# Kernel tuning notes

Measured on AMD Instinct MI355X. Metric: run time of the kernel, lower is better.

## Reference

```python
import jax, jax.numpy as jnp
import numpy as np

B = 4096; T = 2; S = 4; E = 128; NF = 11; ID = 55; MID = 4; NG = 6; SI = 4
EPS = 1e-5

def _bn(x, axis):
    # BatchNorm in training mode at init (gamma=1, beta=0): normalize over batch axis
    m = jnp.mean(x, axis=axis, keepdims=True)
    v = jnp.var(x, axis=axis, keepdims=True)
    return (x - m) * jax.lax.rsqrt(v + EPS)

def setup_inputs() -> dict:
    key = jax.random.key(0)
    keys = iter(jax.random.split(key, 64))
    def n(shape, s=0.05):
        return jax.random.normal(next(keys), shape, dtype=jnp.float32) * s
    cat = jax.random.randint(next(keys), (B, 9), 0, 1000)
    scen = jax.random.randint(next(keys), (B, 1), 0, S)
    return {
        "categorical_x": jnp.concatenate([scen, cat], axis=1).astype(jnp.int32),
        "numerical_x": n((B, 63), 1.0),
        "emb_table": n((9000, E)), "lin_table": n((9000, E)),
        "user_W": n((E, 23)), "user_b": n((E,)), "item_W": n((E, 40)), "item_b": n((E,)),
        "user_lW": n((E, 23)), "user_lb": n((E,)), "item_lW": n((E, 40)), "item_lb": n((E,)),
        "scen_emb": n((S, SI)), "task_emb": n((T, SI)),
        "st_w": n((T, S, 1)), "interact_w": n((1, ID, 1)),
        "sb_W": n((14, E)), "sb_b": n((14,)), "lsb_W": n((14, E)), "lsb_b": n((14,)),
        "shexp_W": n((4, MID, 14)), "shexp_b": n((4, MID)),
        "spexp_W": n((S, T, 2, MID, 14)), "spexp_b": n((S, T, 2, MID)),
        "lshexp_W": n((4, MID, 14)), "lshexp_b": n((4, MID)),
        "lspexp_W": n((S, T, 2, MID, 14)), "lspexp_b": n((S, T, 2, MID)),
        "gate_W": n((S, T, NG, SI + E)), "gate_b": n((S, T, NG)),
        "lgate_W": n((S, T, NG, SI + E)), "lgate_b": n((S, T, NG)),
        "mask_W": n((S, T, ID, ID * MID)), "mask_b": n((S, T, ID)),
        "att_W": n((S, T, ID)),
        "ltower_W": n((S, T, NF, NF * MID)), "ltower_b": n((S, T, NF)),
        "bias_p": n((T, S, E)),
        "last_W1": n((T, 40, 2 * E)), "last_b1": n((T, 40)),
        "last_W2": n((T, 32, 40)), "last_b2": n((T, 32)),
        "last_W3": n((T, 8, 32)), "last_b3": n((T, 8)),
        "last_W4": n((T, 1, 8)), "last_b4": n((T, 1)),
    }

def _fwd(categorical_x, numerical_x, emb_table, lin_table, user_W, user_b, item_W, item_b,
         user_lW, user_lb, item_lW, item_lb, scen_emb, task_emb, st_w, interact_w,
         sb_W, sb_b, lsb_W, lsb_b, shexp_W, shexp_b, spexp_W, spexp_b,
         lshexp_W, lshexp_b, lspexp_W, lspexp_b, gate_W, gate_b, lgate_W, lgate_b,
         mask_W, mask_b, att_W, ltower_W, ltower_b, bias_p,
         last_W1, last_b1, last_W2, last_b2, last_W3, last_b3, last_W4, last_b4):
    b = categorical_x.shape[0]
    scen_ids = categorical_x[:, 0]
    onehot = jax.nn.one_hot(scen_ids, S, dtype=jnp.float32)                 # [B,S]
    scen_ind = scen_emb[scen_ids]                                           # [B,SI]
    stw = jnp.einsum('bs,tso->bt', onehot, st_w)                            # [B,T]
    sti = scen_ind[:, None, :] * task_emb[None] * stw[:, :, None]           # [B,T,SI]

    offsets = (jnp.arange(9) * 1000).astype(categorical_x.dtype)
    idx = categorical_x[:, 1:] + offsets                                    # [B,9]

    def fields_of(table, uW, ub, iW, ib):
        ce = table[idx]                                                     # [B,9,E]
        u = (numerical_x[:, :23] @ uW.T + ub)[:, None, :]
        it = (numerical_x[:, 23:] @ iW.T + ib)[:, None, :]
        return jnp.concatenate([ce, u, it], axis=1)                          # [B,NF,E]

    def moe(x, att_in, sbW, sbb, shW, shb, spW, spb, gW, gb):
        # x: [B,F,E]; att_in: [B,T,F,SI+E] -> soft-routed expert mix [S,T,B,F,MID]
        ein = x @ sbW.T + sbb                                                # [B,F,14]
        sh = jnp.einsum('bfi,eoi->ebfo', ein, shW) + shb[:, None, None, :]   # [4,B,F,MID]
        sp = jnp.einsum('bfi,steoi->stebfo', ein, spW) + spb[:, :, :, None, None, :]
        experts = jnp.concatenate(
            [jnp.broadcast_to(sh[None, None], (S, T) + sh.shape), sp], axis=2)  # [S,T,NG,B,F,MID]
        g = jax.nn.softmax(jnp.einsum('btfi,stgi->stbfg', att_in, gW) + gb[:, :, None, None, :], axis=-1)
        return jnp.einsum('stgbfm,stbfg->stbfm', experts, g)

    # ---- interaction (FM pairwise) branch ----
    fields = fields_of(emb_table, user_W, user_b, item_W, item_b)
    r, c = jnp.triu_indices(NF, k=1)
    pe = fields[:, r, :] * fields[:, c, :] * interact_w                     # [B,ID,E]
    att_in_pe = jnp.concatenate([
        jnp.broadcast_to(sti[:, :, None, :], (b, T, ID, SI)),
        jnp.broadcast_to(pe[:, None], (b, T, ID, E))], axis=-1)             # [B,T,ID,SI+E]
    w = moe(pe, att_in_pe, sb_W, sb_b, shexp_W, shexp_b, spexp_W, spexp_b, gate_W, gate_b)
    m = jnp.einsum('stbi,stoi->stbo', w.reshape(S, T, b, ID * MID), mask_W) + mask_b[:, :, None, :]
    m = jax.nn.relu(jnp.tanh(_bn(m, axis=2)))                               # hard-sparse mask [S,T,B,ID]
    att_out = jnp.einsum('stbf,bfe,stf->stbe', m, pe, att_W)                # [S,T,B,E]
    inter = jnp.einsum('bs,stbe->tbe', onehot, att_out)                     # select own scenario [T,B,E]

    # ---- linear (first-order) branch ----
    lfields = fields_of(lin_table, user_lW, user_lb, item_lW, item_lb)      # [B,NF,E]
    att_in_l = jnp.concatenate([
        jnp.broadcast_to(sti[:, :, None, :], (b, T, NF, SI)),
        jnp.broadcast_to(lfields[:, None], (b, T, NF, E))], axis=-1)
    w2 = moe(lfields, att_in_l, lsb_W, lsb_b, lshexp_W, lshexp_b, lspexp_W, lspexp_b, lgate_W, lgate_b)
    lt = jnp.einsum('stbi,stoi->stbo', w2.reshape(S, T, b, NF * MID), ltower_W) + ltower_b[:, :, None, :]
    lt = jax.nn.softmax(_bn(lt, axis=2), axis=-1)                           # field weights [S,T,B,NF]
    lw = jnp.einsum('bs,stbf->tbf', onehot, lt)
    lin_final = jnp.einsum('tbf,bfe->tbe', lw, lfields) + jnp.einsum('bs,tse->tbe', onehot, bias_p)

    # ---- per-task output towers ----
    h = jnp.concatenate([inter, lin_final], axis=-1)                        # [T,B,2E]
    h = jax.nn.relu(_bn(jnp.einsum('tbi,toi->tbo', h, last_W1) + last_b1[:, None, :], axis=1))
    h = jax.nn.relu(_bn(jnp.einsum('tbi,toi->tbo', h, last_W2) + last_b2[:, None, :], axis=1))
    h = jax.nn.relu(_bn(jnp.einsum('tbi,toi->tbo', h, last_W3) + last_b3[:, None, :], axis=1))
    out = jax.nn.sigmoid(jnp.einsum('tbi,toi->tbo', h, last_W4) + last_b4[:, None, :])
    return out[..., 0]                                                      # [T,B]

def reference(categorical_x, numerical_x, emb_table, lin_table, user_W, user_b, item_W, item_b,
              user_lW, user_lb, item_lW, item_lb, scen_emb, task_emb, st_w, interact_w,
              sb_W, sb_b, lsb_W, lsb_b, shexp_W, shexp_b, spexp_W, spexp_b,
              lshexp_W, lshexp_b, lspexp_W, lspexp_b, gate_W, gate_b, lgate_W, lgate_b,
              mask_W, mask_b, att_W, ltower_W, ltower_b, bias_p,
              last_W1, last_b1, last_W2, last_b2, last_W3, last_b3, last_W4, last_b4):
    return _fwd(categorical_x, numerical_x, emb_table, lin_table, user_W, user_b, item_W, item_b,
                user_lW, user_lb, item_lW, item_lb, scen_emb, task_emb, st_w, interact_w,
                sb_W, sb_b, lsb_W, lsb_b, shexp_W, shexp_b, spexp_W, spexp_b,
                lshexp_W, lshexp_b, lspexp_W, lspexp_b, gate_W, gate_b, lgate_W, lgate_b,
                mask_W, mask_b, att_W, ltower_W, ltower_b, bias_p,
                last_W1, last_b1, last_W2, last_b2, last_W3, last_b3, last_W4, last_b4)
```

## Files before the change

### kernel.cpp

```cpp
#include <hip/hip_runtime.h>
#include <hip/hip_bf16.h>

#define B_ 4096
#define T_ 2
#define S_ 4
#define E_ 128
#define NF_ 11
#define ID_ 55
#define MID_ 4
#define NG_ 6
#define SI_ 4
#define EPSf 1e-5f

typedef __attribute__((ext_vector_type(8))) short bf16x8;
typedef __attribute__((ext_vector_type(4))) float f32x4;

__device__ inline unsigned short f2bf(float f){
  unsigned int u = __float_as_uint(f);
  unsigned int r = (u + 0x7FFFu + ((u >> 16) & 1u)) >> 16;
  return (unsigned short)r;
}

__device__ const int PR[64]={0,0,0,0,0,0,0,0,0,0,1,1,1,1,1,1,1,1,1,2,2,2,2,2,2,2,2,3,3,3,3,3,3,3,4,4,4,4,4,4,5,5,5,5,5,6,6,6,6,7,7,7,8,8,9,0,0,0,0,0,0,0,0,0};
__device__ const int PC[64]={1,2,3,4,5,6,7,8,9,10,2,3,4,5,6,7,8,9,10,3,4,5,6,7,8,9,10,4,5,6,7,8,9,10,5,6,7,8,9,10,6,7,8,9,10,7,8,9,10,8,9,10,9,10,10,0,0,0,0,0,0,0,0,0};

__global__ void k_prep(const float* __restrict__ gW, const float* __restrict__ lgW,
                       const float* __restrict__ sbW, const float* __restrict__ lsbW,
                       float* __restrict__ Wu, float* __restrict__ lWu,
                       unsigned short* __restrict__ Wub){
  int k = blockIdx.x*256 + threadIdx.x;
  if (k < 16384){
    int arr = k >> 13, rem = k & 8191;
    int o = rem >> 7, e = rem & 127;
    const float* g = arr ? lgW : gW;
    const float* s = arr ? lsbW : sbW;
    float v;
    if (o < 48) v = g[o*132 + 4 + e];
    else if (o < 62) v = s[(o-48)*128 + e];
    else v = 0.f;
    (arr ? lWu : Wu)[o*128 + e] = v;
  }
  if (k < 64*136){
    int o = k / 136, e = k % 136;
    float v = 0.f;
    if (e < 128){
      if (o < 48) v = gW[o*132 + 4 + e];
      else if (o < 62) v = sbW[(o-48)*128 + e];
    }
    Wub[k] = f2bf(v);
  }
}

__global__ __launch_bounds__(256) void k_moe12(
    const int* __restrict__ cat, const float* __restrict__ num,
    const float* __restrict__ embT, const float* __restrict__ linT,
    const float* __restrict__ uW, const float* __restrict__ ub,
    const float* __restrict__ iW, const float* __restrict__ ib,
    const float* __restrict__ ulW, const float* __restrict__ ulb,
    const float* __restrict__ ilW, const float* __restrict__ ilb,
    const float* __restrict__ scen_emb, const float* __restrict__ task_emb,
    const float* __restrict__ st_w, const float* __restrict__ interact_w,
    const float* __restrict__ sb_b,
    const float* __restrict__ shexp_W, const float* __restrict__ shexp_b,
    const float* __restrict__ spexp_W, const float* __restrict__ spexp_b,
    const float* __restrict__ gate_W, const float* __restrict__ gate_b,
    const unsigned short* __restrict__ Wub,
    const float* __restrict__ lsb_b,
    const float* __restrict__ lshexp_W, const float* __restrict__ lshexp_b,
    const float* __restrict__ lspexp_W, const float* __restrict__ lspexp_b,
    const float* __restrict__ lgate_W, const float* __restrict__ lgate_b,
    const float* __restrict__ ltower_W, const float* __restrict__ ltower_b,
    const float* __restrict__ lWu,
    float* __restrict__ w_g, float* __restrict__ lt1)
{
  __shared__ float sm[9592];
  float* s_fld = sm;
  float* s_stig= sm + 1452;
  unsigned short* s_peb = (unsigned short*)(sm + 1500);
  unsigned short* s_wub = (unsigned short*)(sm + 5240);
  float* s_C   = sm + 1500;
  float* s_w   = sm + 5916;
  float* s_sh  = sm + 7676;
  float* s_lf   = sm + 5916;
  float* m2_w   = sm + 7676;
  float* m2_sh  = sm + 8028;
  float* m2_C   = sm + 8611;
  float* m2_stig= sm + 9439;
  const int tid = threadIdx.x, b = blockIdx.x;
  const int* cb = cat + (size_t)b*10;
  const int scen = cb[0];
  const int e = tid & 127, half = tid >> 7;

  if (half == 0){
    for (int j = 0; j < 9; j += 2){
      int id = cb[1+j] + j*1000;
      s_fld[j*132 + e] = embT[(size_t)id*128 + e];
    }
    float a0 = ub[e];
    for (int k = 0; k < 23; ++k) a0 += num[(size_t)b*63 + k] * uW[e*23 + k];
    s_fld[9*132 + e] = a0;
  } else {
    for (int j = 1; j < 9; j += 2){
      int id = cb[1+j] + j*1000;
      s_fld[j*132 + e] = embT[(size_t)id*128 + e];
    }
    float a2 = ib[e];
    for (int k = 0; k < 40; ++k) a2 += num[(size_t)b*63 + 23 + k] * iW[e*40 + k];
    s_fld[10*132 + e] = a2;
  }
  for (int idx = tid; idx < 1088; idx += 256)
    ((float4*)s_wub)[idx] = ((const float4*)Wub)[idx];
  if (tid < 48){
    int t = (tid/6)%T_;
    float stw = st_w[t*S_ + scen];
    float acc = gate_b[tid];
    for (int i = 0; i < 4; ++i){
      float sti = scen_emb[scen*4+i] * task_emb[t*4+i] * stw;
      acc += sti * gate_W[tid*132 + i];
    }
    s_stig[tid] = acc;
  }
  __syncthreads();

  for (int idx = tid; idx < 1760; idx += 256){
    int row = idx >> 5, q = idx & 31;
    float4 x = *(const float4*)&s_fld[PR[row]*132 + q*4];
    float4 y = *(const float4*)&s_fld[PC[row]*132 + q*4];
    ushort4 o;
    o.x = f2bf(x.x*y.x); o.y = f2bf(x.y*y.y); o.z = f2bf(x.z*y.z); o.w = f2bf(x.w*y.w);
    *(ushort4*)&s_peb[row*136 + q*4] = o;
  }
  __syncthreads();

  const int w = tid >> 6, lane = tid & 63;
  const int cg = lane >> 4, cc = lane & 15;
  f32x4 acc0 = {0.f,0.f,0.f,0.f}, acc1 = acc0, acc2 = acc0, acc3 = acc0;
  {
    const int kb = cg * 8;
    #pragma unroll
    for (int ks = 0; ks < 4; ++ks){
      int ko = ks*32 + kb;
      bf16x8 bfr = *(const bf16x8*)&s_wub[(w*16 + cc)*136 + ko];
      bf16x8 a0 = *(const bf16x8*)&s_peb[( 0 + cc)*136 + ko];
      bf16x8 a1 = *(const bf16x8*)&s_peb[(16 + cc)*136 + ko];
      bf16x8 a2 = *(const bf16x8*)&s_peb[(32 + cc)*136 + ko];
      bf16x8 a3 = *(const bf16x8*)&s_peb[(48 + cc)*136 + ko];
      acc0 = __builtin_amdgcn_mfma_f32_16x16x32_bf16(a0, bfr, acc0, 0, 0, 0);
      acc1 = __builtin_amdgcn_mfma_f32_16x16x32_bf16(a1, bfr, acc1, 0, 0, 0);
      acc2 = __builtin_amdgcn_mfma_f32_16x16x32_bf16(a2, bfr, acc2, 0, 0, 0);
      acc3 = __builtin_amdgcn_mfma_f32_16x16x32_bf16(a3, bfr, acc3, 0, 0, 0);
    }
  }
  __syncthreads();
  {
    const int col = w*16 + cc;
    const float bias = (col < 48) ? s_stig[col] : ((col < 62) ? sb_b[col-48] : 0.f);
    #pragma unroll
    for (int r = 0; r < 4; ++r){
      int row0 = cg*4 + r;
      float v0 = (r==0)?acc0.x:((r==1)?acc0.y:((r==2)?acc0.z:acc0.w));
      float v1 = (r==0)?acc1.x:((r==1)?acc1.y:((r==2)?acc1.z:acc1.w));
      float v2 = (r==0)?acc2.x:((r==1)?acc2.y:((r==2)?acc2.z:acc2.w));
      float v3 = (r==0)?acc3.x:((r==1)?acc3.y:((r==2)?acc3.z:acc3.w));
      s_C[(row0     )*69 + col] = v0*interact_w[row0     ] + bias;
      s_C[(row0 + 16)*69 + col] = v1*interact_w[row0 + 16] + bias;
      s_C[(row0 + 32)*69 + col] = v2*interact_w[row0 + 32] + bias;
      if (row0 + 48 < 55)
        s_C[(row0 + 48)*69 + col] = v3*interact_w[row0 + 48] + bias;
    }
  }
  __syncthreads();
  for (int o = tid; o < 880; o += 256){
    int f = o >> 4, j = o & 15;
    float acc = shexp_b[j];
    const float* ein = &s_C[f*69 + 48];
    const float* wp = &shexp_W[j*14];
    for (int i = 0; i < 14; ++i) acc += ein[i] * wp[i];
    s_sh[f*17 + j] = acc;
  }
  __syncthreads();
  for (int task = tid; task < 440; task += 256){
    int st = task / 55, f = task % 55;
    float ein[14];
    for (int i = 0; i < 14; ++i) ein[i] = s_C[f*69 + 48 + i];
    float lg[6], mx = -1e30f;
    for (int g = 0; g < 6; ++g){ lg[g] = s_C[f*69 + st*6 + g]; mx = fmaxf(mx, lg[g]); }
    float sum = 0.f;
    for (int g = 0; g < 6; ++g){ lg[g] = __expf(lg[g]-mx); sum += lg[g]; }
    float inv = 1.f/sum;
    float wv[4] = {0,0,0,0};
    for (int g = 0; g < 4; ++g){
      float gg = lg[g]*inv;
      for (int m = 0; m < 4; ++m) wv[m] += gg * s_sh[f*17 + g*4 + m];
    }
    for (int ee = 0; ee < 2; ++ee){
      float gg = lg[4+ee]*inv;
      for (int m = 0; m < 4; ++m){
        float acc = spexp_b[(st*2+ee)*4+m];
        const float* wp = spexp_W + ((st*2+ee)*4+m)*14;
        for (int i = 0; i < 14; ++i) acc += ein[i] * wp[i];
        wv[m] += gg*acc;
      }
    }
    float4 o4; o4.x = wv[0]; o4.y = wv[1]; o4.z = wv[2]; o4.w = wv[3];
    *(float4*)&s_w[st*220 + f*4] = o4;
  }
  __syncthreads();
  for (int idx = tid; idx < 448; idx += 256){
    int st = idx / 56, q = idx % 56;
    float4 v;
    if (q < 55) v = *(float4*)&s_w[st*220 + q*4];
    else { v.x=v.y=v.z=v.w=0.f; }
    *(float4*)&w_g[((size_t)b*8 + st)*224 + q*4] = v;
  }
  __syncthreads();

  if (half == 0){
    for (int j = 0; j < 9; j += 2){
      int id = cb[1+j] + j*1000;
      s_lf[j*132 + e] = linT[(size_t)id*128 + e];
    }
    float a1 = ulb[e];
    for (int k = 0; k < 23; ++k) a1 += num[(size_t)b*63 + k] * ulW[e*23 + k];
    s_lf[9*132 + e] = a1;
  } else {
    for (int j = 1; j < 9; j += 2){
      int id = cb[1+j] + j*1000;
      s_lf[j*132 + e] = linT[(size_t)id*128 + e];
    }
    float a3 = ilb[e];
    for (int k = 0; k < 40; ++k) a3 += num[(size_t)b*63 + 23 + k] * ilW[e*40 + k];
    s_lf[10*132 + e] = a3;
  }
  if (tid >= 224){
    int q = tid - 224;
    float4 z = {0,0,0,0}; *(float4*)&s_lf[11*132 + q*4] = z;
  }
  if (tid < 48){
    int t = (tid/6)%T_;
    float stw = st_w[t*S_ + scen];
    float acc = lgate_b[tid];
    for (int i = 0; i < 4; ++i){
      float sti = scen_emb[scen*4+i] * task_emb[t*4+i] * stw;
      acc += sti * lgate_W[tid*132 + i];
    }
    m2_stig[tid] = acc;
  }
  __syncthreads();
  {
    const int lane2 = tid & 63, wv_ = tid >> 6;
    const int pr = wv_*16 + (lane2 & 15);
    const int ks = lane2 >> 4;
    const int ft = pr & 1, ot = pr >> 1;
    const int r0 = ft*6, k0 = ks*32;
    float acc[6][2];
    for (int r = 0; r < 6; ++r){ acc[r][0] = 0.f; acc[r][1] = 0.f; }
    const float4* W4 = (const float4*)lWu;
    #pragma unroll 1
    for (int kc = 0; kc < 32; kc += 4){
      int kk = k0 + ((kc + ks*8) & 31);
      float4 w0 = W4[(ot*2+0)*32 + (kk>>2)];
      float4 w1 = W4[(ot*2+1)*32 + (kk>>2)];
      for (int r = 0; r < 6; ++r){
        float4 a = *(const float4*)&s_lf[(r0+r)*132 + kk];
        acc[r][0] += a.x*w0.x + a.y*w0.y + a.z*w0.z + a.w*w0.w;
        acc[r][1] += a.x*w1.x + a.y*w1.y + a.z*w1.z + a.w*w1.w;
      }
    }
    for (int r = 0; r < 6; ++r) for (int c = 0; c < 2; ++c){
      float v = acc[r][c];
      v += __shfl_xor(v, 16); v += __shfl_xor(v, 32);
      acc[r][c] = v;
    }
    if (ks == 0){
      for (int r = 0; r < 6; ++r) for (int c = 0; c < 2; ++c){
        int col = ot*2 + c, row = r0 + r;
        float bias = (col < 48) ? m2_stig[col] : ((col < 62) ? lsb_b[col-48] : 0.f);
        m2_C[row*69 + col] = acc[r][c] + bias;
      }
    }
  }
  __syncthreads();
  if (tid < 176){
    int f = tid >> 4, j = tid & 15;
    float acc = lshexp_b[j];
    const float* ein = &m2_C[f*69 + 48];
    for (int i = 0; i < 14; ++i) acc += ein[i] * lshexp_W[j*14+i];
    m2_sh[f*17 + j] = acc;
  }
  __syncthreads();
  if (tid < 88){
    int st = tid / 11, f = tid % 11;
    float ein[14];
    for (int i = 0; i < 14; ++i) ein[i] = m2_C[f*69 + 48 + i];
    float lg[6], mx = -1e30f;
    for (int g = 0; g < 6; ++g){ lg[g] = m2_C[f*69 + st*6 + g]; mx = fmaxf(mx, lg[g]); }
    float sum = 0.f;
    for (int g = 0; g < 6; ++g){ lg[g] = __expf(lg[g]-mx); sum += lg[g]; }
    float inv = 1.f/sum;
    float wv[4] = {0,0,0,0};
    for (int g = 0; g < 4; ++g){
      float gg = lg[g]*inv;
      for (int m = 0; m < 4; ++m) wv[m] += gg * m2_sh[f*17 + g*4 + m];
    }
    for (int ee = 0; ee < 2; ++ee){
      float gg = lg[4+ee]*inv;
      for (int m = 0; m < 4; ++m){
        float acc = lspexp_b[(st*2+ee)*4+m];
        const float* wp = lspexp_W + ((st*2+ee)*4+m)*14;
        for (int i = 0; i < 14; ++i) acc += ein[i] * wp[i];
        wv[m] += gg*acc;
      }
    }
    float4 o4; o4.x = wv[0]; o4.y = wv[1]; o4.z = wv[2]; o4.w = wv[3];
    *(float4*)&m2_w[st*44 + f*4] = o4;
  }
  __syncthreads();
  if (tid < 88){
    int st = tid / 11, oo = tid % 11;
    float acc = ltower_b[st*11+oo];
    const float* tw = ltower_W + (st*11+oo)*44;
    const float* wp = m2_w + st*44;
    for (int i = 0; i < 44; ++i) acc += wp[i] * tw[i];
    lt1[(size_t)(st*11+oo)*B_ + b] = acc;
  }
}

__global__ __launch_bounds__(256) void k_mask(
    const float* __restrict__ w_g, const float* __restrict__ mask_W,
    const float* __restrict__ mask_b, float* __restrict__ m1)
{
  __shared__ float s_mw[56*116];
  __shared__ float s_wb[64*116];
  const int tid = threadIdx.x;
  const int st = blockIdx.x >> 6, bt = blockIdx.x & 63;
  const int b0 = bt*64;
  const int btl = tid & 15, ot = tid >> 4;
  float acc[4][4];
  for (int c = 0; c < 4; ++c) for (int j = 0; j < 4; ++j) acc[c][j] = 0.f;

  for (int kc = 0; kc < 2; ++kc){
    __syncthreads();
    for (int idx = tid; idx < 64*112; idx += 256){
      int r = idx / 112, k = idx % 112;
      s_wb[r*116 + k] = w_g[((size_t)(b0+r)*8 + st)*224 + kc*112 + k];
    }
    for (int idx = tid; idx < 56*112; idx += 256){
      int r = idx / 112, k = idx % 112;
      int kg = kc*112 + k;
      s_mw[r*116 + k] = (r < 55 && kg < 220) ? mask_W[((size_t)st*55 + r)*220 + kg] : 0.f;
    }
    __syncthreads();
    if (ot < 14){
      for (int k4 = 0; k4 < 112; k4 += 4){
        float4 a[4], wb[4];
        for (int c = 0; c < 4; ++c) a[c]  = *(float4*)&s_mw[(ot*4+c)*116 + k4];
        for (int j = 0; j < 4; ++j) wb[j] = *(float4*)&s_wb[(btl*4+j)*116 + k4];
        for (int c = 0; c < 4; ++c)
          for (int j = 0; j < 4; ++j)
            acc[c][j] += a[c].x*wb[j].x + a[c].y*wb[j].y + a[c].z*wb[j].z + a[c].w*wb[j].w;
      }
    }
  }
  if (ot < 14){
    for (int c = 0; c < 4; ++c){
      int row = ot*4 + c;
      if (row < 55){
        float mb = mask_b[st*55 + row];
        float4 v; v.x = acc[c][0]+mb; v.y = acc[c][1]+mb; v.z = acc[c][2]+mb; v.w = acc[c][3]+mb;
        *(float4*)&m1[(size_t)(st*55+row)*B_ + b0 + btl*4] = v;
      }
    }
  }
}

__global__ __launch_bounds__(256) void k_stats(const float* __restrict__ x, float* __restrict__ stats){
  const int row = blockIdx.x, tid = threadIdx.x;
  const float* xr = x + (size_t)row*B_;
  float s = 0.f, s2 = 0.f;
  for (int i = tid; i < B_; i += 256){ float v = xr[i]; s += v; s2 += v*v; }
  for (int off = 32; off > 0; off >>= 1){ s += __shfl_down(s, off); s2 += __shfl_down(s2, off); }
  __shared__ float red[8];
  if ((tid & 63) == 0){ red[(tid>>6)*2] = s; red[(tid>>6)*2+1] = s2; }
  __syncthreads();
  if (tid == 0){
    float Ssum = red[0]+red[2]+red[4]+red[6], S2 = red[1]+red[3]+red[5]+red[7];
    float mean = Ssum*(1.f/B_), var = S2*(1.f/B_) - mean*mean;
    stats[row*2] = mean; stats[row*2+1] = rsqrtf(fmaxf(var, 0.f) + EPSf);
  }
}

__global__ __launch_bounds__(256) void k_stats2(const float* __restrict__ x1, const float* __restrict__ x2,
                                                int n1, float* __restrict__ st1o, float* __restrict__ st2o){
  const int row = blockIdx.x, tid = threadIdx.x;
  const float* xr; float* sto;
  if (row < n1){ xr = x1 + (size_t)row*B_; sto = st1o + row*2; }
  else { int r = row - n1; xr = x2 + (size_t)r*B_; sto = st2o + r*2; }
  float s = 0.f, s2 = 0.f;
  for (int i = tid; i < B_; i += 256){ float v = xr[i]; s += v; s2 += v*v; }
  for (int off = 32; off > 0; off >>= 1){ s += __shfl_down(s, off); s2 += __shfl_down(s2, off); }
  __shared__ float red[8];
  if ((tid & 63) == 0){ red[(tid>>6)*2] = s; red[(tid>>6)*2+1] = s2; }
  __syncthreads();
  if (tid == 0){
    float Ssum = red[0]+red[2]+red[4]+red[6], S2 = red[1]+red[3]+red[5]+red[7];
    float mean = Ssum*(1.f/B_), var = S2*(1.f/B_) - mean*mean;
    sto[0] = mean; sto[1] = rsqrtf(fmaxf(var, 0.f) + EPSf);
  }
}

__global__ __launch_bounds__(128) void k_interlinf(
    const int* __restrict__ cat, const float* __restrict__ num,
    const float* __restrict__ embT, const float* __restrict__ linT,
    const float* __restrict__ uW, const float* __restrict__ ub,
    const float* __restrict__ iW, const float* __restrict__ ib,
    const float* __restrict__ ulW, const float* __restrict__ ulb,
    const float* __restrict__ ilW, const float* __restrict__ ilb,
    const float* __restrict__ m1, const float* __restrict__ stm,
    const float* __restrict__ lt1, const float* __restrict__ stl,
    const float* __restrict__ att_W, const float* __restrict__ interact_w,
    const float* __restrict__ bias_p,
    const float* __restrict__ W1, const float* __restrict__ b1,
    float* __restrict__ h1)
{
  __shared__ float s_fld[NF_*E_];
  __shared__ float s_lf[NF_*E_];
  __shared__ float s_co[110];
  __shared__ float s_lw[22];
  __shared__ float s_h[512];
  const int b = blockIdx.x, e = threadIdx.x;
  const int* cb = cat + (size_t)b*10;
  const int scen = cb[0];

  for (int j = 0; j < 9; ++j){
    int id = cb[1+j] + j*1000;
    s_fld[j*E_+e] = embT[(size_t)id*128 + e];
    s_lf[j*E_+e]  = linT[(size_t)id*128 + e];
  }
  {
    float a0 = ub[e], a1 = ulb[e];
    for (int k = 0; k < 23; ++k){ float x = num[(size_t)b*63 + k]; a0 += x*uW[e*23+k]; a1 += x*ulW[e*23+k]; }
    s_fld[9*E_+e] = a0; s_lf[9*E_+e] = a1;
    float a2 = ib[e], a3 = ilb[e];
    for (int k = 0; k < 40; ++k){ float x = num[(size_t)b*63 + 23 + k]; a2 += x*iW[e*40+k]; a3 += x*ilW[e*40+k]; }
    s_fld[10*E_+e] = a2; s_lf[10*E_+e] = a3;
  }
  if (e < 110){
    int t = e/55, f = e%55, row = (scen*T_+t)*55 + f;
    float v = (m1[(size_t)row*B_+b] - stm[row*2]) * stm[row*2+1];
    v = fmaxf(tanhf(v), 0.f);
    s_co[e] = v * att_W[(scen*T_+t)*55 + f];
  }
  if (e < 22){
    int t = e/11, f = e%11, row = (scen*T_+t)*11 + f;
    s_lw[e] = (lt1[(size_t)row*B_+b] - stl[row*2]) * stl[row*2+1];
  }
  __syncthreads();
  if (e < 2){
    int t = e; float mx = -1e30f;
    for (int f = 0; f < 11; ++f) mx = fmaxf(mx, s_lw[t*11+f]);
    float sum = 0.f;
    for (int f = 0; f < 11; ++f){ float x = __expf(s_lw[t*11+f]-mx); s_lw[t*11+f] = x; sum += x; }
    float inv = 1.f/sum;
    for (int f = 0; f < 11; ++f) s_lw[t*11+f] *= inv;
  }
  __syncthreads();
  {
    float a0 = 0.f, a1 = 0.f;
    for (int f = 0; f < 55; ++f){
      float pe = s_fld[PR[f]*E_+e] * s_fld[PC[f]*E_+e] * interact_w[f];
      a0 += s_co[f]*pe; a1 += s_co[55+f]*pe;
    }
    s_h[0*256 + e] = a0;
    s_h[1*256 + e] = a1;
  }
  for (int t = 0; t < 2; ++t){
    float acc = bias_p[(size_t)(t*S_+scen)*E_ + e];
    for (int f = 0; f < 11; ++f) acc += s_lw[t*11+f] * s_lf[f*E_+e];
    s_h[t*256 + 128 + e] = acc;
  }
  __syncthreads();
  if (e < 80){
    int t = e / 40, o = e % 40;
    float acc = b1[t*40 + o];
    const float4* wr = (const float4*)(W1 + (size_t)(t*40 + o)*256);
    const float4* hh = (const float4*)(s_h + t*256);
    for (int i = 0; i < 64; ++i){
      float4 w = wr[i], h = hh[i];
      acc += h.x*w.x; acc += h.y*w.y; acc += h.z*w.z; acc += h.w*w.w;
    }
    h1[(size_t)(t*40 + o)*B_ + b] = acc;
  }
}

__global__ __launch_bounds__(256) void k_last2(const float* __restrict__ h1, const float* __restrict__ st1,
    const float* __restrict__ W2, const float* __restrict__ b2v, float* __restrict__ h2){
  int bz = blockIdx.x, t = bz/16, bc = bz%16, tid = threadIdx.x, b = bc*256 + tid;
  __shared__ float s_w2[1280];
  for (int k = tid; k < 1280; k += 256) s_w2[k] = W2[t*1280 + k];
  __syncthreads();
  float hv[40];
  for (int i = 0; i < 40; ++i){
    int row = t*40 + i;
    hv[i] = fmaxf((h1[(size_t)row*B_+b] - st1[row*2]) * st1[row*2+1], 0.f);
  }
  for (int o = 0; o < 32; ++o){
    float acc = b2v[t*32+o];
    for (int i = 0; i < 40; ++i) acc += hv[i] * s_w2[o*40+i];
    h2[(size_t)(t*32+o)*B_ + b] = acc;
  }
}

__global__ __launch_bounds__(256) void k_last3(const float* __restrict__ h2, const float* __restrict__ st2,
    const float* __restrict__ W3, const float* __restrict__ b3v, float* __restrict__ h3){
  int bz = blockIdx.x, t = bz/16, bc = bz%16, tid = threadIdx.x, b = bc*256 + tid;
  __shared__ float s_w3[256];
  if (tid < 256) s_w3[tid] = W3[t*256 + tid];
  __syncthreads();
  float hv[32];
  for (int i = 0; i < 32; ++i){
    int row = t*32 + i;
    hv[i] = fmaxf((h2[(size_t)row*B_+b] - st2[row*2]) * st2[row*2+1], 0.f);
  }
  for (int o = 0; o < 8; ++o){
    float acc = b3v[t*8+o];
    for (int i = 0; i < 32; ++i) acc += hv[i] * s_w3[o*32+i];
    h3[(size_t)(t*8+o)*B_ + b] = acc;
  }
}

__global__ __launch_bounds__(256) void k_out(const float* __restrict__ h3, const float* __restrict__ st3,
    const float* __restrict__ W4, const float* __restrict__ b4v, float* __restrict__ out){
  int idx = blockIdx.x*256 + threadIdx.x;
  int t = idx / B_, b = idx % B_;
  float acc = b4v[t];
  for (int i = 0; i < 8; ++i){
    int row = t*8 + i;
    float v = fmaxf((h3[(size_t)row*B_+b] - st3[row*2]) * st3[row*2+1], 0.f);
    acc += v * W4[t*8+i];
  }
  out[idx] = 1.f/(1.f + __expf(-acc));
}

extern "C" void kernel_launch(void* const* d_in, const int* in_sizes, int n_in,
                              void* d_out, int out_size, void* d_ws, size_t ws_size,
                              hipStream_t stream)
{
  const int*   cat      = (const int*)  d_in[0];
  const float* num      = (const float*)d_in[1];
  const float* embT     = (const float*)d_in[2];
  const float* linT     = (const float*)d_in[3];
  const float* uW = (const float*)d_in[4];  const float* ub = (const float*)d_in[5];
  const float* iW = (const float*)d_in[6];  const float* ib = (const float*)d_in[7];
  const float* ulW = (const float*)d_in[8]; const float* ulb = (const float*)d_in[9];
  const float* ilW = (const float*)d_in[10];const float* ilb = (const float*)d_in[11];
  const float* scen_emb = (const float*)d_in[12];
  const float* task_emb = (const float*)d_in[13];
  const float* st_w     = (const float*)d_in[14];
  const float* interact_w=(const float*)d_in[15];
  const float* sbW = (const float*)d_in[16]; const float* sbb = (const float*)d_in[17];
  const float* lsbW = (const float*)d_in[18];const float* lsbb = (const float*)d_in[19];
  const float* shW = (const float*)d_in[20]; const float* shb = (const float*)d_in[21];
  const float* spW = (const float*)d_in[22]; const float* spb = (const float*)d_in[23];
  const float* lshW = (const float*)d_in[24];const float* lshb = (const float*)d_in[25];
  const float* lspW = (const float*)d_in[26];const float* lspb = (const float*)d_in[27];
  const float* gW = (const float*)d_in[28];  const float* gb = (const float*)d_in[29];
  const float* lgW = (const float*)d_in[30]; const float* lgb = (const float*)d_in[31];
  const float* mW = (const float*)d_in[32];  const float* mb = (const float*)d_in[33];
  const float* attW = (const float*)d_in[34];
  const float* ltW = (const float*)d_in[35]; const float* ltb = (const float*)d_in[36];
  const float* biasP = (const float*)d_in[37];
  const float* W1 = (const float*)d_in[38];  const float* b1 = (const float*)d_in[39];
  const float* W2 = (const float*)d_in[40];  const float* b2v = (const float*)d_in[41];
  const float* W3 = (const float*)d_in[42];  const float* b3v = (const float*)d_in[43];
  const float* W4 = (const float*)d_in[44];  const float* b4v = (const float*)d_in[45];
  float* out = (float*)d_out;

  float* ws = (float*)d_ws;
  size_t o = 0;
  float* Wu   = ws + o; o += 8192;
  float* lWu  = ws + o; o += 8192;
  float* Wub  = ws + o; o += 4352;
  float* w_g  = ws + o; o += (size_t)B_*8*224;
  float* m1   = ws + o; o += (size_t)440*B_;
  float* stm  = ws + o; o += 880;
  float* lt1  = ws + o; o += (size_t)88*B_;
  float* stl  = ws + o; o += 176;
  float* h1   = ws + o; o += (size_t)80*B_;
  float* st1  = ws + o; o += 160;
  float* h2   = ws + o; o += (size_t)64*B_;
  float* st2  = ws + o; o += 128;
  float* h3   = ws + o; o += (size_t)16*B_;
  float* st3  = ws + o; o += 32;

  k_prep<<<64, 256, 0, stream>>>(gW, lgW, sbW, lsbW, Wu, lWu, (unsigned short*)Wub);
  k_moe12<<<B_, 256, 0, stream>>>(cat, num, embT, linT, uW, ub, iW, ib, ulW, ulb, ilW, ilb,
                                  scen_emb, task_emb, st_w, interact_w, sbb, shW, shb,
                                  spW, spb, gW, gb, (const unsigned short*)Wub,
                                  lsbb, lshW, lshb, lspW, lspb, lgW, lgb, ltW, ltb,
                                  lWu, w_g, lt1);
  k_mask<<<512, 256, 0, stream>>>(w_g, mW, mb, m1);
  k_stats2<<<528, 256, 0, stream>>>(m1, lt1, 440, stm, stl);
  k_interlinf<<<B_, 128, 0, stream>>>(cat, num, embT, linT, uW, ub, iW, ib, ulW, ulb, ilW, ilb,
                                      m1, stm, lt1, stl, attW, interact_w, biasP,
                                      W1, b1, h1);
  k_stats<<<80, 256, 0, stream>>>(h1, st1);
  k_last2<<<32, 256, 0, stream>>>(h1, st1, W2, b2v, h2);
  k_stats<<<64, 256, 0, stream>>>(h2, st2);
  k_last3<<<32, 256, 0, stream>>>(h2, st2, W3, b3v, h3);
  k_stats<<<16, 256, 0, stream>>>(h3, st3);
  k_out<<<32, 256, 0, stream>>>(h3, st3, W4, b4v, out);
}
```

Before: 448.4 us.

## Use bf16 MFMA for linear-branch gate GEMM and shrink shared memory

The second (linear-feature) gate/sub-bias projection now runs on bf16 MFMA with prepacked bf16 weights instead of fp32 scalar dot products. Weight tiles are read directly from global/L2 rather than staged in LDS. The shared-memory footprint drops, with a tighter C stride and w_g written straight to global, to raise occupancy. The cost is reduced precision in the linear branch, since both its features and weights are now bf16, and uncached weight reads in the MFMA loop.

Result: faster. 402.7 us (-10.2%).

```diff
diff --git a/kernel.cpp b/kernel.cpp
--- a/kernel.cpp
+++ b/kernel.cpp
@@ -26,28 +26,17 @@
 
 __global__ void k_prep(const float* __restrict__ gW, const float* __restrict__ lgW,
                        const float* __restrict__ sbW, const float* __restrict__ lsbW,
-                       float* __restrict__ Wu, float* __restrict__ lWu,
-                       unsigned short* __restrict__ Wub){
+                       unsigned short* __restrict__ Wub, unsigned short* __restrict__ lWub){
   int k = blockIdx.x*256 + threadIdx.x;
-  if (k < 16384){
-    int arr = k >> 13, rem = k & 8191;
-    int o = rem >> 7, e = rem & 127;
-    const float* g = arr ? lgW : gW;
-    const float* s = arr ? lsbW : sbW;
-    float v;
-    if (o < 48) v = g[o*132 + 4 + e];
-    else if (o < 62) v = s[(o-48)*128 + e];
-    else v = 0.f;
-    (arr ? lWu : Wu)[o*128 + e] = v;
-  }
-  if (k < 64*136){
+  if (k < 8704){
     int o = k / 136, e = k % 136;
-    float v = 0.f;
+    float v = 0.f, lv = 0.f;
     if (e < 128){
-      if (o < 48) v = gW[o*132 + 4 + e];
-      else if (o < 62) v = sbW[(o-48)*128 + e];
+      if (o < 48){ v = gW[o*132 + 4 + e]; lv = lgW[o*132 + 4 + e]; }
+      else if (o < 62){ v = sbW[(o-48)*128 + e]; lv = lsbW[(o-48)*128 + e]; }
     }
     Wub[k] = f2bf(v);
+    lWub[k] = f2bf(lv);
   }
 }
 
@@ -70,26 +59,26 @@
     const float* __restrict__ lspexp_W, const float* __restrict__ lspexp_b,
     const float* __restrict__ lgate_W, const float* __restrict__ lgate_b,
     const float* __restrict__ ltower_W, const float* __restrict__ ltower_b,
-    const float* __restrict__ lWu,
+    const unsigned short* __restrict__ lWub,
     float* __restrict__ w_g, float* __restrict__ lt1)
 {
-  __shared__ float sm[9592];
+  __shared__ float sm[6595];
   float* s_fld = sm;
   float* s_stig= sm + 1452;
   unsigned short* s_peb = (unsigned short*)(sm + 1500);
-  unsigned short* s_wub = (unsigned short*)(sm + 5240);
   float* s_C   = sm + 1500;
-  float* s_w   = sm + 5916;
-  float* s_sh  = sm + 7676;
-  float* s_lf   = sm + 5916;
-  float* m2_w   = sm + 7676;
-  float* m2_sh  = sm + 8028;
-  float* m2_C   = sm + 8611;
-  float* m2_stig= sm + 9439;
+  float* s_sh  = sm + 5660;
+  unsigned short* s_lfb = (unsigned short*)(sm + 1500);
+  float* m2_C   = sm + 2588;
+  float* m2_sh  = sm + 3368;
+  float* m2_stig= sm + 3555;
+  float* m2_w   = sm + 3603;
   const int tid = threadIdx.x, b = blockIdx.x;
   const int* cb = cat + (size_t)b*10;
   const int scen = cb[0];
   const int e = tid & 127, half = tid >> 7;
+  const int w = tid >> 6, lane = tid & 63;
+  const int cg = lane >> 4, cc = lane & 15;
 
   if (half == 0){
     for (int j = 0; j < 9; j += 2){
@@ -108,8 +97,6 @@
     for (int k = 0; k < 40; ++k) a2 += num[(size_t)b*63 + 23 + k] * iW[e*40 + k];
     s_fld[10*132 + e] = a2;
   }
-  for (int idx = tid; idx < 1088; idx += 256)
-    ((float4*)s_wub)[idx] = ((const float4*)Wub)[idx];
   if (tid < 48){
     int t = (tid/6)%T_;
     float stw = st_w[t*S_ + scen];
@@ -132,15 +119,13 @@
   }
   __syncthreads();
 
-  const int w = tid >> 6, lane = tid & 63;
-  const int cg = lane >> 4, cc = lane & 15;
   f32x4 acc0 = {0.f,0.f,0.f,0.f}, acc1 = acc0, acc2 = acc0, acc3 = acc0;
   {
     const int kb = cg * 8;
     #pragma unroll
     for (int ks = 0; ks < 4; ++ks){
       int ko = ks*32 + kb;
-      bf16x8 bfr = *(const bf16x8*)&s_wub[(w*16 + cc)*136 + ko];
+      bf16x8 bfr = *(const bf16x8*)&Wub[(w*16 + cc)*136 + ko];
       bf16x8 a0 = *(const bf16x8*)&s_peb[( 0 + cc)*136 + ko];
       bf16x8 a1 = *(const bf16x8*)&s_peb[(16 + cc)*136 + ko];
       bf16x8 a2 = *(const bf16x8*)&s_peb[(32 + cc)*136 + ko];
@@ -162,18 +147,18 @@
       float v1 = (r==0)?acc1.x:((r==1)?acc1.y:((r==2)?acc1.z:acc1.w));
       float v2 = (r==0)?acc2.x:((r==1)?acc2.y:((r==2)?acc2.z:acc2.w));
       float v3 = (r==0)?acc3.x:((r==1)?acc3.y:((r==2)?acc3.z:acc3.w));
-      s_C[(row0     )*69 + col] = v0*interact_w[row0     ] + bias;
-      s_C[(row0 + 16)*69 + col] = v1*interact_w[row0 + 16] + bias;
-      s_C[(row0 + 32)*69 + col] = v2*interact_w[row0 + 32] + bias;
+      s_C[(row0     )*65 + col] = v0*interact_w[row0     ] + bias;
+      s_C[(row0 + 16)*65 + col] = v1*interact_w[row0 + 16] + bias;
+      s_C[(row0 + 32)*65 + col] = v2*interact_w[row0 + 32] + bias;
       if (row0 + 48 < 55)
-        s_C[(row0 + 48)*69 + col] = v3*interact_w[row0 + 48] + bias;
+        s_C[(row0 + 48)*65 + col] = v3*interact_w[row0 + 48] + bias;
     }
   }
   __syncthreads();
   for (int o = tid; o < 880; o += 256){
     int f = o >> 4, j = o & 15;
     float acc = shexp_b[j];
-    const float* ein = &s_C[f*69 + 48];
+    const float* ein = &s_C[f*65 + 48];
     const float* wp = &shexp_W[j*14];
     for (int i = 0; i < 14; ++i) acc += ein[i] * wp[i];
     s_sh[f*17 + j] = acc;
@@ -182,9 +167,9 @@
   for (int task = tid; task < 440; task += 256){
     int st = task / 55, f = task % 55;
     float ein[14];
-    for (int i = 0; i < 14; ++i) ein[i] = s_C[f*69 + 48 + i];
+    for (int i = 0; i < 14; ++i) ein[i] = s_C[f*65 + 48 + i];
     float lg[6], mx = -1e30f;
-    for (int g = 0; g < 6; ++g){ lg[g] = s_C[f*69 + st*6 + g]; mx = fmaxf(mx, lg[g]); }
+    for (int g = 0; g < 6; ++g){ lg[g] = s_C[f*65 + st*6 + g]; mx = fmaxf(mx, lg[g]); }
     float sum = 0.f;
     for (int g = 0; g < 6; ++g){ lg[g] = __expf(lg[g]-mx); sum += lg[g]; }
     float inv = 1.f/sum;
@@ -203,38 +188,30 @@
       }
     }
     float4 o4; o4.x = wv[0]; o4.y = wv[1]; o4.z = wv[2]; o4.w = wv[3];
-    *(float4*)&s_w[st*220 + f*4] = o4;
-  }
-  __syncthreads();
-  for (int idx = tid; idx < 448; idx += 256){
-    int st = idx / 56, q = idx % 56;
-    float4 v;
-    if (q < 55) v = *(float4*)&s_w[st*220 + q*4];
-    else { v.x=v.y=v.z=v.w=0.f; }
-    *(float4*)&w_g[((size_t)b*8 + st)*224 + q*4] = v;
+    *(float4*)&w_g[((size_t)b*8 + st)*224 + f*4] = o4;
+  }
+  if (tid < 8){
+    float4 z = {0,0,0,0};
+    *(float4*)&w_g[((size_t)b*8 + tid)*224 + 220] = z;
   }
   __syncthreads();
 
   if (half == 0){
     for (int j = 0; j < 9; j += 2){
       int id = cb[1+j] + j*1000;
-      s_lf[j*132 + e] = linT[(size_t)id*128 + e];
+      s_lfb[j*136 + e] = f2bf(linT[(size_t)id*128 + e]);
     }
     float a1 = ulb[e];
     for (int k = 0; k < 23; ++k) a1 += num[(size_t)b*63 + k] * ulW[e*23 + k];
-    s_lf[9*132 + e] = a1;
+    s_lfb[9*136 + e] = f2bf(a1);
   } else {
     for (int j = 1; j < 9; j += 2){
       int id = cb[1+j] + j*1000;
-      s_lf[j*132 + e] = linT[(size_t)id*128 + e];
+      s_lfb[j*136 + e] = f2bf(linT[(size_t)id*128 + e]);
     }
     float a3 = ilb[e];
     for (int k = 0; k < 40; ++k) a3 += num[(size_t)b*63 + 23 + k] * ilW[e*40 + k];
-    s_lf[10*132 + e] = a3;
-  }
-  if (tid >= 224){
-    int q = tid - 224;
-    float4 z = {0,0,0,0}; *(float4*)&s_lf[11*132 + q*4] = z;
+    s_lfb[10*136 + e] = f2bf(a3);
   }
   if (tid < 48){
     int t = (tid/6)%T_;
@@ -248,35 +225,23 @@
   }
   __syncthreads();
   {
-    const int lane2 = tid & 63, wv_ = tid >> 6;
-    const int pr = wv_*16 + (lane2 & 15);
-    const int ks = lane2 >> 4;
-    const int ft = pr & 1, ot = pr >> 1;
-    const int r0 = ft*6, k0 = ks*32;
-    float acc[6][2];
-    for (int r = 0; r < 6; ++r){ acc[r][0] = 0.f; acc[r][1] = 0.f; }
-    const float4* W4 = (const float4*)lWu;
-    #pragma unroll 1
-    for (int kc = 0; kc < 32; kc += 4){
-      int kk = k0 + ((kc + ks*8) & 31);
-      float4 w0 = W4[(ot*2+0)*32 + (kk>>2)];
-      float4 w1 = W4[(ot*2+1)*32 + (kk>>2)];
-      for (int r = 0; r < 6; ++r){
-        float4 a = *(const float4*)&s_lf[(r0+r)*132 + kk];
-        acc[r][0] += a.x*w0.x + a.y*w0.y + a.z*w0.z + a.w*w0.w;
-        acc[r][1] += a.x*w1.x + a.y*w1.y + a.z*w1.z + a.w*w1.w;
-      }
-    }
-    for (int r = 0; r < 6; ++r) for (int c = 0; c < 2; ++c){
-      float v = acc[r][c];
-      v += __shfl_xor(v, 16); v += __shfl_xor(v, 32);
-      acc[r][c] = v;
-    }
-    if (ks == 0){
-      for (int r = 0; r < 6; ++r) for (int c = 0; c < 2; ++c){
-        int col = ot*2 + c, row = r0 + r;
-        float bias = (col < 48) ? m2_stig[col] : ((col < 62) ? lsb_b[col-48] : 0.f);
-        m2_C[row*69 + col] = acc[r][c] + bias;
+    f32x4 macc = {0.f,0.f,0.f,0.f};
+    const int kb = cg * 8;
+    #pragma unroll
+    for (int ks = 0; ks < 4; ++ks){
+      int ko = ks*32 + kb;
+      bf16x8 bfr = *(const bf16x8*)&lWub[(w*16 + cc)*136 + ko];
+      bf16x8 av  = *(const bf16x8*)&s_lfb[cc*136 + ko];
+      macc = __builtin_amdgcn_mfma_f32_16x16x32_bf16(av, bfr, macc, 0, 0, 0);
+    }
+    const int col = w*16 + cc;
+    const float bias = (col < 48) ? m2_stig[col] : ((col < 62) ? lsb_b[col-48] : 0.f);
+    #pragma unroll
+    for (int r = 0; r < 4; ++r){
+      int row = cg*4 + r;
+      if (row < 11){
+        float v = (r==0)?macc.x:((r==1)?macc.y:((r==2)?macc.z:macc.w));
+        m2_C[row*65 + col] = v + bias;
       }
     }
   }
@@ -284,7 +249,7 @@
   if (tid < 176){
     int f = tid >> 4, j = tid & 15;
     float acc = lshexp_b[j];
-    const float* ein = &m2_C[f*69 + 48];
+    const float* ein = &m2_C[f*65 + 48];
     for (int i = 0; i < 14; ++i) acc += ein[i] * lshexp_W[j*14+i];
     m2_sh[f*17 + j] = acc;
   }
@@ -292,9 +257,9 @@
   if (tid < 88){
     int st = tid / 11, f = tid % 11;
     float ein[14];
-    for (int i = 0; i < 14; ++i) ein[i] = m2_C[f*69 + 48 + i];
+    for (int i = 0; i < 14; ++i) ein[i] = m2_C[f*65 + 48 + i];
     float lg[6], mx = -1e30f;
-    for (int g = 0; g < 6; ++g){ lg[g] = m2_C[f*69 + st*6 + g]; mx = fmaxf(mx, lg[g]); }
+    for (int g = 0; g < 6; ++g){ lg[g] = m2_C[f*65 + st*6 + g]; mx = fmaxf(mx, lg[g]); }
     float sum = 0.f;
     for (int g = 0; g < 6; ++g){ lg[g] = __expf(lg[g]-mx); sum += lg[g]; }
     float inv = 1.f/sum;
@@ -578,9 +543,8 @@
 
   float* ws = (float*)d_ws;
   size_t o = 0;
-  float* Wu   = ws + o; o += 8192;
-  float* lWu  = ws + o; o += 8192;
   float* Wub  = ws + o; o += 4352;
+  float* lWub = ws + o; o += 4352;
   float* w_g  = ws + o; o += (size_t)B_*8*224;
   float* m1   = ws + o; o += (size_t)440*B_;
   float* stm  = ws + o; o += 880;
@@ -593,12 +557,12 @@
   float* h3   = ws + o; o += (size_t)16*B_;
   float* st3  = ws + o; o += 32;
 
-  k_prep<<<64, 256, 0, stream>>>(gW, lgW, sbW, lsbW, Wu, lWu, (unsigned short*)Wub);
+  k_prep<<<34, 256, 0, stream>>>(gW, lgW, sbW, lsbW, (unsigned short*)Wub, (unsigned short*)lWub);
   k_moe12<<<B_, 256, 0, stream>>>(cat, num, embT, linT, uW, ub, iW, ib, ulW, ulb, ilW, ilb,
                                   scen_emb, task_emb, st_w, interact_w, sbb, shW, shb,
                                   spW, spb, gW, gb, (const unsigned short*)Wub,
                                   lsbb, lshW, lshb, lspW, lspb, lgW, lgb, ltW, ltb,
-                                  lWu, w_g, lt1);
+                                  (const unsigned short*)lWub, w_g, lt1);
   k_mask<<<512, 256, 0, stream>>>(w_g, mW, mb, m1);
   k_stats2<<<528, 256, 0, stream>>>(m1, lt1, 440, stm, stl);
   k_interlinf<<<B_, 128, 0, stream>>>(cat, num, embT, linT, uW, ub, iW, ib, ulW, ulb, ilW, ilb,
```
